# Kernel optimization log

Measured on AMD Instinct MI355X. Metric: run time of the kernel, lower is better.

## Reference

```python
import jax, jax.numpy as jnp
import numpy as np

BC = 48
DIM = 192


def setup_inputs() -> dict:
    key = jax.random.key(0)
    ks = jax.random.split(key, 10)
    s = 0.05
    return {
        "input": jax.random.normal(ks[0], (1, BC, DIM, DIM), jnp.float32),
        "qw": jax.random.normal(ks[1], (BC // 3, BC), jnp.float32) * s,
        "qb": jax.random.normal(ks[2], (BC // 3,), jnp.float32) * s,
        "kw": jax.random.normal(ks[3], (BC // 3, BC), jnp.float32) * s,
        "kb": jax.random.normal(ks[4], (BC // 3,), jnp.float32) * s,
        "vw": jax.random.normal(ks[5], (BC, BC), jnp.float32) * s,
        "vb": jax.random.normal(ks[6], (BC,), jnp.float32) * s,
        "gamma": jnp.float32(0.1),  # torch init is 0.0; nonzero to exercise attn path
        "dw": jax.random.normal(ks[7], (BC, BC, 4, 4), jnp.float32) * s,  # torch ConvTranspose2d [in,out,kh,kw]
        "db": jax.random.normal(ks[8], (BC,), jnp.float32) * s,
    }


def reference(input, qw, qb, kw, kb, vw, vb, gamma, dw, db):
    B, C, H, W = input.shape  # B == 1
    x = input.reshape(B, C, H // 2, 2, W // 2, 2).mean(axis=(3, 5))
    h, w = H // 2, W // 2
    n = h * w
    f = x.reshape(1, C, n)
    # 1x1 Conv1d == per-position linear over channels
    q = jnp.einsum('oc,bcn->bno', qw, f) + qb            # [1, N, bc//3]
    k = jnp.einsum('oc,bcn->bon', kw, f) + kb[:, None]    # [1, bc//3, N]
    v = jnp.einsum('oc,bcn->bon', vw, f) + vb[:, None]    # [1, bc, N]
    qk = jnp.einsum('bno,bom->bnm', q, k)                 # [1, N, N]
    attn = jax.nn.softmax(qk, axis=1)                     # softmax over QUERY axis (dim 1), as in source
    o = jnp.einsum('bcn,bnm->bcm', v, attn)               # [1, bc, N]
    out = gamma * o.reshape(x.shape) + x
    # ConvTranspose2d(k=4, s=2, p=1): conv with lhs_dilation=2, pad k-1-p=2, flipped kernel
    kern = jnp.flip(jnp.transpose(dw, (1, 0, 2, 3)), axis=(2, 3))  # [out, in, kh, kw]
    y = jax.lax.conv_general_dilated(
        out, kern, window_strides=(1, 1), padding=((2, 2), (2, 2)),
        lhs_dilation=(2, 2), dimension_numbers=('NCHW', 'OIHW', 'NCHW'))
    return y + db[None, :, None, None]
```

## Files before the change

### kernel.cpp

```cpp
#include <hip/hip_runtime.h>
#include <hip/hip_bf16.h>

#define C 48
#define HH 192
#define WW 192
#define HP 96
#define WP 96
#define NP 9216

#define OFF_QB    0
#define OFF_KB    36864
#define OFF_VT2   73728
#define OFF_PART  368640
#define OFF_XT    5087232
#define OFF_XTP   5529600
#define OFF_WB    5836928
#define WS_NEED_BYTES ((size_t)5861504 * 4)

typedef __attribute__((ext_vector_type(4))) short s16x4;
typedef __attribute__((ext_vector_type(8))) short s16x8;
typedef __attribute__((ext_vector_type(4))) float f32x4;

#if __has_builtin(__builtin_amdgcn_mfma_f32_16x16x16bf16_1k)
static __device__ inline f32x4 mfma16(s16x4 a, s16x4 b, f32x4 c) {
    return __builtin_amdgcn_mfma_f32_16x16x16bf16_1k(a, b, c, 0, 0, 0);
}
#else
static __device__ inline f32x4 mfma16(s16x4 a, s16x4 b, f32x4 c) {
    asm volatile("v_mfma_f32_16x16x16_bf16 %0, %1, %2, %0" : "+v"(c) : "v"(a), "v"(b));
    return c;
}
#endif

static __device__ inline f32x4 mfma32(s16x8 a, s16x8 b, f32x4 c) {
    return __builtin_amdgcn_mfma_f32_16x16x32_bf16(a, b, c, 0, 0, 0);
}

static __device__ inline float fexp2(float x) {
    float r;
    asm("v_exp_f32 %0, %1" : "=v"(r) : "v"(x));
    return r;
}

static __device__ inline unsigned short f2bf(float f) {
    union { float f; unsigned u; } v; v.f = f;
    unsigned r = v.u + 0x7fff + ((v.u >> 16) & 1);
    return (unsigned short)(r >> 16);
}

static __device__ inline float bf2f(unsigned short u) {
    union { unsigned u; float f; } v; v.u = ((unsigned)u) << 16; return v.f;
}

static __device__ inline s16x4 pack_bf16x4(float a, float b, float c, float d) {
    __hip_bfloat162 h0 = __float22bfloat162_rn(make_float2(a, b));
    __hip_bfloat162 h1 = __float22bfloat162_rn(make_float2(c, d));
    union { unsigned u[2]; s16x4 v; } pu;
    pu.u[0] = *reinterpret_cast<unsigned*>(&h0);
    pu.u[1] = *reinterpret_cast<unsigned*>(&h1);
    return pu.v;
}

__global__ void pool_k(const float* __restrict__ in, float* __restrict__ xT) {
    int idx = blockIdx.x * 256 + threadIdx.x;
    if (idx >= C * NP) return;
    int c = idx / NP, r = idx % NP;
    int y = r / WP, xx = r % WP;
    const float* p = in + (size_t)c * HH * WW + (2 * y) * WW + 2 * xx;
    xT[(size_t)r * 48 + c] = 0.25f * (p[0] + p[1] + p[WW] + p[WW + 1]);
}

__global__ void qkvprep_k(const float* __restrict__ xT,
                          const float* __restrict__ qw, const float* __restrict__ qb,
                          const float* __restrict__ kw, const float* __restrict__ kb,
                          const float* __restrict__ vw, const float* __restrict__ vb,
                          unsigned short* __restrict__ QB, unsigned short* __restrict__ KB,
                          unsigned short* __restrict__ VT2) {
    int tid = blockIdx.x * 256 + threadIdx.x;
    int p = tid % NP;
    int g = tid / NP;
    float f[C];
#pragma unroll
    for (int c4 = 0; c4 < C; c4 += 4) {
        f32x4 v = *(const f32x4*)(xT + (size_t)p * 48 + c4);
        f[c4] = v[0]; f[c4 + 1] = v[1]; f[c4 + 2] = v[2]; f[c4 + 3] = v[3];
    }
    int nt = p >> 4, nn = p & 15;
    if (g == 0) {
#pragma unroll
        for (int o = 0; o < 16; ++o) {
            float a = qb[o];
#pragma unroll
            for (int c = 0; c < C; ++c) a += qw[o * C + c] * f[c];
            QB[p * 16 + o] = f2bf(a);
        }
    } else if (g == 1) {
        const float L2E = 1.4426950408889634f;
#pragma unroll
        for (int o = 0; o < 16; ++o) {
            float a = kb[o];
#pragma unroll
            for (int c = 0; c < C; ++c) a += kw[o * C + c] * f[c];
            KB[p * 16 + o] = f2bf(a * L2E);
        }
        VT2[(size_t)nt * 1024 + 48 * 16 + nn] = 0x3F80;
#pragma unroll
        for (int r = 49; r < 64; ++r) VT2[(size_t)nt * 1024 + r * 16 + nn] = 0;
    } else {
        int c0 = (g - 2) * 16;
#pragma unroll
        for (int oo = 0; oo < 16; ++oo) {
            int o = c0 + oo;
            float a = vb[o];
#pragma unroll
            for (int c = 0; c < C; ++c) a += vw[o * C + c] * f[c];
            VT2[(size_t)nt * 1024 + o * 16 + nn] = f2bf(a);
        }
    }
}

#define MBLKS 72
#define NSPL  16
#define NSTEP 36

static __device__ __forceinline__ void attn_core(const unsigned short* __restrict__ QB,
                                                 const unsigned short* __restrict__ VT2,
                                                 s16x4 bq0, s16x4 bq1, int n0, int lo, int hi,
                                                 f32x4 o0[4], f32x4 o1[4]) {
    const unsigned short* qp = QB + (size_t)(n0 + lo) * 16 + 4 * hi;
    const unsigned short* vp = VT2 + (size_t)(n0 >> 4) * 1024 + lo * 16 + 4 * hi;

    s16x4 aq  = *(const s16x4*)qp;
    s16x4 bv0 = *(const s16x4*)(vp);
    s16x4 bv1 = *(const s16x4*)(vp + 256);
    s16x4 bv2 = *(const s16x4*)(vp + 512);
    s16x4 bv3 = *(const s16x4*)(vp + 768);

    for (int s = 0; s < NSTEP; ++s) {
        qp += 16 * 16;
        vp += 1024;
        s16x4 aqn  = *(const s16x4*)qp;
        s16x4 bvn0 = *(const s16x4*)(vp);
        s16x4 bvn1 = *(const s16x4*)(vp + 256);
        s16x4 bvn2 = *(const s16x4*)(vp + 512);
        s16x4 bvn3 = *(const s16x4*)(vp + 768);

        f32x4 z = {0.f, 0.f, 0.f, 0.f};
        f32x4 t0 = mfma16(aq, bq0, z);
        f32x4 t1 = mfma16(aq, bq1, z);

        s16x4 p0 = pack_bf16x4(fexp2(t0[0]), fexp2(t0[1]), fexp2(t0[2]), fexp2(t0[3]));
        s16x4 p1 = pack_bf16x4(fexp2(t1[0]), fexp2(t1[1]), fexp2(t1[2]), fexp2(t1[3]));

        o0[0] = mfma16(p0, bv0, o0[0]);
        o0[1] = mfma16(p0, bv1, o0[1]);
        o0[2] = mfma16(p0, bv2, o0[2]);
        o0[3] = mfma16(p0, bv3, o0[3]);
        o1[0] = mfma16(p1, bv0, o1[0]);
        o1[1] = mfma16(p1, bv1, o1[1]);
        o1[2] = mfma16(p1, bv2, o1[2]);
        o1[3] = mfma16(p1, bv3, o1[3]);

        aq = aqn; bv0 = bvn0; bv1 = bvn1; bv2 = bvn2; bv3 = bvn3;
    }
}

__global__ __launch_bounds__(256) void attn_k(const unsigned short* __restrict__ QB,
                                              const unsigned short* __restrict__ KB,
                                              const unsigned short* __restrict__ VT2,
                                              unsigned short* __restrict__ PART) {
    const int lane = threadIdx.x & 63;
    const int lo = lane & 15, hi = lane >> 4;
    const int wv = threadIdx.x >> 6;
    const int mblk = blockIdx.x % MBLKS;
    const int nspl = blockIdx.x / MBLKS;
    const int mt0 = mblk * 128 + wv * 32;

    const s16x4 bq0 = *(const s16x4*)(KB + (size_t)(mt0 + lo) * 16 + 4 * hi);
    const s16x4 bq1 = *(const s16x4*)(KB + (size_t)(mt0 + 16 + lo) * 16 + 4 * hi);

    f32x4 o0[4], o1[4];
#pragma unroll
    for (int i = 0; i < 4; ++i) {
        o0[i] = (f32x4){0.f, 0.f, 0.f, 0.f};
        o1[i] = (f32x4){0.f, 0.f, 0.f, 0.f};
    }
    attn_core(QB, VT2, bq0, bq1, nspl * (NP / NSPL), lo, hi, o0, o1);

    unsigned short* cp = PART + ((size_t)(mblk * 4 + wv) * NSPL + nspl) * 2048;
#pragma unroll
    for (int q = 0; q < 8; ++q) {
        const f32x4& o = (q >> 2) ? o1[q & 3] : o0[q & 3];
        s16x4 pk = pack_bf16x4(o[0], o[1], o[2], o[3]);
        *(s16x4*)(cp + q * 256 + lane * 4) = pk;
    }
}

__global__ __launch_bounds__(256) void reduce_epi_k(const unsigned short* __restrict__ PART,
                                                    const float* __restrict__ xT,
                                                    const float* __restrict__ gamma,
                                                    unsigned short* __restrict__ XTP) {
    __shared__ float sden[32];
    const int T = blockIdx.x;
    const int mt0 = (T >> 2) * 128 + (T & 3) * 32;
    const unsigned short* base = PART + (size_t)T * NSPL * 2048;
    const int t = threadIdx.x;

    if (t < 8) {
        int h = t >> 2, hi = t & 3;
        int idx = (h * 4 + 3) * 256 + (hi * 16) * 4;
        float a0 = 0.f, a1 = 0.f, a2 = 0.f, a3 = 0.f;
        for (int ns = 0; ns < NSPL; ++ns) {
            s16x4 v = *(const s16x4*)(base + ns * 2048 + idx);
            a0 += bf2f((unsigned short)v[0]);
            a1 += bf2f((unsigned short)v[1]);
            a2 += bf2f((unsigned short)v[2]);
            a3 += bf2f((unsigned short)v[3]);
        }
        sden[h * 16 + hi * 4 + 0] = a0;
        sden[h * 16 + hi * 4 + 1] = a1;
        sden[h * 16 + hi * 4 + 2] = a2;
        sden[h * 16 + hi * 4 + 3] = a3;
    }
    __syncthreads();

    float gam = gamma[0];
#pragma unroll
    for (int g = t; g < 512; g += 256) {
        int q = g >> 6, lane = g & 63;
        int h = q >> 2, ct = q & 3;
        int hi = lane >> 4, lo = lane & 15;
        int c = ct * 16 + lo;
        int idx = q * 256 + lane * 4;
        float a0 = 0.f, a1 = 0.f, a2 = 0.f, a3 = 0.f;
        for (int ns = 0; ns < NSPL; ++ns) {
            s16x4 v = *(const s16x4*)(base + ns * 2048 + idx);
            a0 += bf2f((unsigned short)v[0]);
            a1 += bf2f((unsigned short)v[1]);
            a2 += bf2f((unsigned short)v[2]);
            a3 += bf2f((unsigned short)v[3]);
        }
        if (c < 48) {
            float av[4] = {a0, a1, a2, a3};
#pragma unroll
            for (int j = 0; j < 4; ++j) {
                int ml = h * 16 + hi * 4 + j;
                int m = mt0 + ml;
                float val = gam * av[j] / sden[ml] + xT[(size_t)m * 48 + c];
                int iy = m / WP, ix = m % WP;
                XTP[((size_t)(iy + 1) * 98 + ix + 1) * 64 + c] = f2bf(val);
            }
        }
    }
}

__global__ __launch_bounds__(256) void attn_atomic_k(const unsigned short* __restrict__ QB,
                                                     const unsigned short* __restrict__ KB,
                                                     const unsigned short* __restrict__ VT2,
                                                     float* __restrict__ O4) {
    const int lane = threadIdx.x & 63;
    const int lo = lane & 15, hi = lane >> 4;
    const int wv = threadIdx.x >> 6;
    const int mblk = blockIdx.x % MBLKS;
    const int nspl = blockIdx.x / MBLKS;
    const int mt0 = mblk * 128 + wv * 32;

    const s16x4 bq0 = *(const s16x4*)(KB + (size_t)(mt0 + lo) * 16 + 4 * hi);
    const s16x4 bq1 = *(const s16x4*)(KB + (size_t)(mt0 + 16 + lo) * 16 + 4 * hi);

    f32x4 o0[4], o1[4];
#pragma unroll
    for (int i = 0; i < 4; ++i) {
        o0[i] = (f32x4){0.f, 0.f, 0.f, 0.f};
        o1[i] = (f32x4){0.f, 0.f, 0.f, 0.f};
    }
    attn_core(QB, VT2, bq0, bq1, nspl * (NP / NSPL), lo, hi, o0, o1);

    float* Oc = O4 + (size_t)(nspl & 3) * (NP * 64);
#pragma unroll
    for (int ct = 0; ct < 4; ++ct)
#pragma unroll
        for (int j = 0; j < 4; ++j) {
            atomicAdd(&Oc[(size_t)(mt0 + 4 * hi + j) * 64 + 16 * ct + lo], o0[ct][j]);
            atomicAdd(&Oc[(size_t)(mt0 + 16 + 4 * hi + j) * 64 + 16 * ct + lo], o1[ct][j]);
        }
}

__global__ void epi_atomic_k(const float* __restrict__ O4, const float* __restrict__ xT,
                             const float* __restrict__ gamma, unsigned short* __restrict__ XTP) {
    int m = blockIdx.x * 256 + threadIdx.x;
    if (m >= NP) return;
    int iy = m / WP, ix = m % WP;
    unsigned short* xp = XTP + ((size_t)(iy + 1) * 98 + ix + 1) * 64;
    float den = 0.f;
#pragma unroll
    for (int cp = 0; cp < 4; ++cp) den += O4[(size_t)cp * (NP * 64) + (size_t)m * 64 + 48];
    float rg = gamma[0] / den;
#pragma unroll
    for (int c = 0; c < C; ++c) {
        float o = 0.f;
#pragma unroll
        for (int cp = 0; cp < 4; ++cp) o += O4[(size_t)cp * (NP * 64) + (size_t)m * 64 + c];
        xp[c] = f2bf(rg * o + xT[(size_t)m * 48 + c]);
    }
}

__global__ void wprep_k(const float* __restrict__ dw, unsigned short* __restrict__ WB) {
    int idx = blockIdx.x * 256 + threadIdx.x;
    if (idx >= 16 * 48 * 64) return;
    int ci = idx & 63;
    int co = (idx >> 6) % 48;
    int kidx = idx / (48 * 64);
    float v = (ci < C) ? dw[((size_t)ci * C + co) * 16 + kidx] : 0.f;
    WB[idx] = f2bf(v);
}

__global__ __launch_bounds__(128) void convt_mfma_k(const unsigned short* __restrict__ XTP,
                                                    const unsigned short* __restrict__ WB,
                                                    const float* __restrict__ db,
                                                    float* __restrict__ y) {
    const int lane = threadIdx.x & 63;
    const int lo = lane & 15, hi = lane >> 4;
    const int wv = threadIdx.x >> 6;
    const int b = blockIdx.x;
    const int oyp = b >> 2;
    const int py = (b >> 1) & 1;
    const int px = b & 1;

    const int sy[2] = {0, py ? 1 : -1};
    const int kyt[2] = {py ? 2 : 1, py ? 0 : 3};
    const int sx[2] = {0, px ? 1 : -1};
    const int kxt[2] = {px ? 2 : 1, px ? 0 : 3};

    s16x8 bw[2][2][2][3];
#pragma unroll
    for (int ty = 0; ty < 2; ++ty)
#pragma unroll
        for (int tx = 0; tx < 2; ++tx) {
            const unsigned short* wp = WB + (size_t)(kyt[ty] * 4 + kxt[tx]) * 48 * 64;
#pragma unroll
            for (int kk = 0; kk < 2; ++kk)
#pragma unroll
                for (int ct = 0; ct < 3; ++ct)
                    bw[ty][tx][kk][ct] = *(const s16x8*)(wp + (size_t)(ct * 16 + lo) * 64 + kk * 32 + 8 * hi);
        }
    float bias[3];
#pragma unroll
    for (int ct = 0; ct < 3; ++ct) bias[ct] = db[ct * 16 + lo];

    const int oy = 2 * oyp + py;
    for (int i = 0; i < 3; ++i) {
        int ox0 = (wv * 3 + i) * 16;
        f32x4 acc[3];
#pragma unroll
        for (int ct = 0; ct < 3; ++ct) acc[ct] = (f32x4){bias[ct], bias[ct], bias[ct], bias[ct]};
#pragma unroll
        for (int ty = 0; ty < 2; ++ty) {
            int R0 = (oyp + sy[ty] + 1) * 98;
#pragma unroll
            for (int tx = 0; tx < 2; ++tx) {
                const unsigned short* ap = XTP + (size_t)(R0 + ox0 + sx[tx] + 1 + lo) * 64 + 8 * hi;
#pragma unroll
                for (int kk = 0; kk < 2; ++kk) {
                    s16x8 a = *(const s16x8*)(ap + kk * 32);
                    acc[0] = mfma32(a, bw[ty][tx][kk][0], acc[0]);
                    acc[1] = mfma32(a, bw[ty][tx][kk][1], acc[1]);
                    acc[2] = mfma32(a, bw[ty][tx][kk][2], acc[2]);
                }
            }
        }
#pragma unroll
        for (int ct = 0; ct < 3; ++ct)
#pragma unroll
            for (int j = 0; j < 4; ++j)
                y[(size_t)(ct * 16 + lo) * (HH * WW) + oy * WW + 2 * (ox0 + 4 * hi + j) + px] = acc[ct][j];
    }
}

extern "C" void kernel_launch(void* const* d_in, const int* in_sizes, int n_in,
                              void* d_out, int out_size, void* d_ws, size_t ws_size,
                              hipStream_t stream) {
    const float* in    = (const float*)d_in[0];
    const float* qw    = (const float*)d_in[1];
    const float* qb    = (const float*)d_in[2];
    const float* kw    = (const float*)d_in[3];
    const float* kb    = (const float*)d_in[4];
    const float* vw    = (const float*)d_in[5];
    const float* vb    = (const float*)d_in[6];
    const float* gamma = (const float*)d_in[7];
    const float* dw    = (const float*)d_in[8];
    const float* db    = (const float*)d_in[9];
    float* out = (float*)d_out;

    float* ws = (float*)d_ws;
    unsigned short* QB   = (unsigned short*)(ws + OFF_QB);
    unsigned short* KB   = (unsigned short*)(ws + OFF_KB);
    unsigned short* VT2  = (unsigned short*)(ws + OFF_VT2);
    unsigned short* PART = (unsigned short*)(ws + OFF_PART);
    float*          xT   = ws + OFF_XT;
    unsigned short* XTP  = (unsigned short*)(ws + OFF_XTP);
    unsigned short* WB   = (unsigned short*)(ws + OFF_WB);

    pool_k<<<(C * NP + 255) / 256, 256, 0, stream>>>(in, xT);
    qkvprep_k<<<(5 * NP) / 256, 256, 0, stream>>>(xT, qw, qb, kw, kb, vw, vb, QB, KB, VT2);
    hipMemsetAsync(XTP, 0, (size_t)98 * 98 * 64 * sizeof(unsigned short), stream);
    wprep_k<<<(16 * 48 * 64) / 256, 256, 0, stream>>>(dw, WB);

    if (ws_size >= WS_NEED_BYTES) {
        attn_k<<<MBLKS * NSPL, 256, 0, stream>>>(QB, KB, VT2, PART);
        reduce_epi_k<<<288, 256, 0, stream>>>(PART, xT, gamma, XTP);
    } else {
        float* O4 = (float*)PART;
        hipMemsetAsync(O4, 0, (size_t)4 * NP * 64 * sizeof(float), stream);
        attn_atomic_k<<<MBLKS * NSPL, 256, 0, stream>>>(QB, KB, VT2, O4);
        epi_atomic_k<<<(NP + 255) / 256, 256, 0, stream>>>(O4, xT, gamma, XTP);
    }
    convt_mfma_k<<<96 * 2 * 2, 128, 0, stream>>>(XTP, WB, db, out);
}
```

Baseline: 85.98 us.

## Widen attention tiles to 64 keys per wave and zero only XTP border

The attention kernel now has each wave cover 64 key positions (four 16-row tiles) instead of 32, so every Q/V fragment it loads feeds twice as many MFMAs. The query range is split 32 ways instead of 16, and the reduction kernel is reshaped to match (144 blocks over 64 positions each). The full memset of the padded XTP buffer is replaced by writing zeros only to its one-pixel border inside wprep_k. In exchange it uses twice the accumulator registers, which may lower occupancy, and needs a larger partials buffer, so the atomic fallback runs when the workspace is too small.

```diff
diff --git a/kernel.cpp b/kernel.cpp
--- a/kernel.cpp
+++ b/kernel.cpp
@@ -11,11 +11,12 @@
 #define OFF_QB    0
 #define OFF_KB    36864
 #define OFF_VT2   73728
-#define OFF_PART  368640
-#define OFF_XT    5087232
-#define OFF_XTP   5529600
-#define OFF_WB    5836928
-#define WS_NEED_BYTES ((size_t)5861504 * 4)
+#define OFF_XT    368640
+#define OFF_XTP   811008
+#define OFF_WB    1118336
+#define OFF_PART  1142912
+#define WS_NEED_BYTES ((size_t)10580096 * 4)
+#define FB_NEED_BYTES ((size_t)3502208 * 4)
 
 typedef __attribute__((ext_vector_type(4))) short s16x4;
 typedef __attribute__((ext_vector_type(8))) short s16x8;
@@ -119,51 +120,9 @@
     }
 }
 
-#define MBLKS 72
-#define NSPL  16
-#define NSTEP 36
-
-static __device__ __forceinline__ void attn_core(const unsigned short* __restrict__ QB,
-                                                 const unsigned short* __restrict__ VT2,
-                                                 s16x4 bq0, s16x4 bq1, int n0, int lo, int hi,
-                                                 f32x4 o0[4], f32x4 o1[4]) {
-    const unsigned short* qp = QB + (size_t)(n0 + lo) * 16 + 4 * hi;
-    const unsigned short* vp = VT2 + (size_t)(n0 >> 4) * 1024 + lo * 16 + 4 * hi;
-
-    s16x4 aq  = *(const s16x4*)qp;
-    s16x4 bv0 = *(const s16x4*)(vp);
-    s16x4 bv1 = *(const s16x4*)(vp + 256);
-    s16x4 bv2 = *(const s16x4*)(vp + 512);
-    s16x4 bv3 = *(const s16x4*)(vp + 768);
-
-    for (int s = 0; s < NSTEP; ++s) {
-        qp += 16 * 16;
-        vp += 1024;
-        s16x4 aqn  = *(const s16x4*)qp;
-        s16x4 bvn0 = *(const s16x4*)(vp);
-        s16x4 bvn1 = *(const s16x4*)(vp + 256);
-        s16x4 bvn2 = *(const s16x4*)(vp + 512);
-        s16x4 bvn3 = *(const s16x4*)(vp + 768);
-
-        f32x4 z = {0.f, 0.f, 0.f, 0.f};
-        f32x4 t0 = mfma16(aq, bq0, z);
-        f32x4 t1 = mfma16(aq, bq1, z);
-
-        s16x4 p0 = pack_bf16x4(fexp2(t0[0]), fexp2(t0[1]), fexp2(t0[2]), fexp2(t0[3]));
-        s16x4 p1 = pack_bf16x4(fexp2(t1[0]), fexp2(t1[1]), fexp2(t1[2]), fexp2(t1[3]));
-
-        o0[0] = mfma16(p0, bv0, o0[0]);
-        o0[1] = mfma16(p0, bv1, o0[1]);
-        o0[2] = mfma16(p0, bv2, o0[2]);
-        o0[3] = mfma16(p0, bv3, o0[3]);
-        o1[0] = mfma16(p1, bv0, o1[0]);
-        o1[1] = mfma16(p1, bv1, o1[1]);
-        o1[2] = mfma16(p1, bv2, o1[2]);
-        o1[3] = mfma16(p1, bv3, o1[3]);
-
-        aq = aqn; bv0 = bvn0; bv1 = bvn1; bv2 = bvn2; bv3 = bvn3;
-    }
-}
+#define MBLKS 36
+#define NSPL  32
+#define NSTEP 18
 
 __global__ __launch_bounds__(256) void attn_k(const unsigned short* __restrict__ QB,
                                               const unsigned short* __restrict__ KB,
@@ -174,67 +133,119 @@
     const int wv = threadIdx.x >> 6;
     const int mblk = blockIdx.x % MBLKS;
     const int nspl = blockIdx.x / MBLKS;
-    const int mt0 = mblk * 128 + wv * 32;
-
-    const s16x4 bq0 = *(const s16x4*)(KB + (size_t)(mt0 + lo) * 16 + 4 * hi);
-    const s16x4 bq1 = *(const s16x4*)(KB + (size_t)(mt0 + 16 + lo) * 16 + 4 * hi);
-
-    f32x4 o0[4], o1[4];
-#pragma unroll
-    for (int i = 0; i < 4; ++i) {
-        o0[i] = (f32x4){0.f, 0.f, 0.f, 0.f};
-        o1[i] = (f32x4){0.f, 0.f, 0.f, 0.f};
-    }
-    attn_core(QB, VT2, bq0, bq1, nspl * (NP / NSPL), lo, hi, o0, o1);
-
-    unsigned short* cp = PART + ((size_t)(mblk * 4 + wv) * NSPL + nspl) * 2048;
-#pragma unroll
-    for (int q = 0; q < 8; ++q) {
-        const f32x4& o = (q >> 2) ? o1[q & 3] : o0[q & 3];
-        s16x4 pk = pack_bf16x4(o[0], o[1], o[2], o[3]);
-        *(s16x4*)(cp + q * 256 + lane * 4) = pk;
-    }
+    const int mt0 = mblk * 256 + wv * 64;
+
+    s16x4 bq0 = *(const s16x4*)(KB + (size_t)(mt0 + lo) * 16 + 4 * hi);
+    s16x4 bq1 = *(const s16x4*)(KB + (size_t)(mt0 + 16 + lo) * 16 + 4 * hi);
+    s16x4 bq2 = *(const s16x4*)(KB + (size_t)(mt0 + 32 + lo) * 16 + 4 * hi);
+    s16x4 bq3 = *(const s16x4*)(KB + (size_t)(mt0 + 48 + lo) * 16 + 4 * hi);
+
+    f32x4 o[4][4];
+#pragma unroll
+    for (int mt = 0; mt < 4; ++mt)
+#pragma unroll
+        for (int ct = 0; ct < 4; ++ct) o[mt][ct] = (f32x4){0.f, 0.f, 0.f, 0.f};
+
+    const int n0 = nspl * (NP / NSPL);
+    const unsigned short* qp = QB + (size_t)(n0 + lo) * 16 + 4 * hi;
+    const unsigned short* vp = VT2 + (size_t)(n0 >> 4) * 1024 + lo * 16 + 4 * hi;
+
+    s16x4 aq  = *(const s16x4*)qp;
+    s16x4 bv0 = *(const s16x4*)(vp);
+    s16x4 bv1 = *(const s16x4*)(vp + 256);
+    s16x4 bv2 = *(const s16x4*)(vp + 512);
+    s16x4 bv3 = *(const s16x4*)(vp + 768);
+
+    for (int s = 0; s < NSTEP; ++s) {
+        qp += 256;
+        vp += 1024;
+        s16x4 aqn  = *(const s16x4*)qp;
+        s16x4 bvn0 = *(const s16x4*)(vp);
+        s16x4 bvn1 = *(const s16x4*)(vp + 256);
+        s16x4 bvn2 = *(const s16x4*)(vp + 512);
+        s16x4 bvn3 = *(const s16x4*)(vp + 768);
+
+        f32x4 z = {0.f, 0.f, 0.f, 0.f};
+        f32x4 t0 = mfma16(aq, bq0, z);
+        f32x4 t1 = mfma16(aq, bq1, z);
+        f32x4 t2 = mfma16(aq, bq2, z);
+        f32x4 t3 = mfma16(aq, bq3, z);
+
+        s16x4 p0 = pack_bf16x4(fexp2(t0[0]), fexp2(t0[1]), fexp2(t0[2]), fexp2(t0[3]));
+        s16x4 p1 = pack_bf16x4(fexp2(t1[0]), fexp2(t1[1]), fexp2(t1[2]), fexp2(t1[3]));
+        s16x4 p2 = pack_bf16x4(fexp2(t2[0]), fexp2(t2[1]), fexp2(t2[2]), fexp2(t2[3]));
+        s16x4 p3 = pack_bf16x4(fexp2(t3[0]), fexp2(t3[1]), fexp2(t3[2]), fexp2(t3[3]));
+
+        o[0][0] = mfma16(p0, bv0, o[0][0]);
+        o[0][1] = mfma16(p0, bv1, o[0][1]);
+        o[0][2] = mfma16(p0, bv2, o[0][2]);
+        o[0][3] = mfma16(p0, bv3, o[0][3]);
+        o[1][0] = mfma16(p1, bv0, o[1][0]);
+        o[1][1] = mfma16(p1, bv1, o[1][1]);
+        o[1][2] = mfma16(p1, bv2, o[1][2]);
+        o[1][3] = mfma16(p1, bv3, o[1][3]);
+        o[2][0] = mfma16(p2, bv0, o[2][0]);
+        o[2][1] = mfma16(p2, bv1, o[2][1]);
+        o[2][2] = mfma16(p2, bv2, o[2][2]);
+        o[2][3] = mfma16(p2, bv3, o[2][3]);
+        o[3][0] = mfma16(p3, bv0, o[3][0]);
+        o[3][1] = mfma16(p3, bv1, o[3][1]);
+        o[3][2] = mfma16(p3, bv2, o[3][2]);
+        o[3][3] = mfma16(p3, bv3, o[3][3]);
+
+        aq = aqn; bv0 = bvn0; bv1 = bvn1; bv2 = bvn2; bv3 = bvn3;
+    }
+
+    unsigned short* cp = PART + ((size_t)(mblk * 4 + wv) * NSPL + nspl) * 4096;
+#pragma unroll
+    for (int mt = 0; mt < 4; ++mt)
+#pragma unroll
+        for (int ct = 0; ct < 4; ++ct) {
+            int q = mt * 4 + ct;
+            s16x4 pk = pack_bf16x4(o[mt][ct][0], o[mt][ct][1], o[mt][ct][2], o[mt][ct][3]);
+            *(s16x4*)(cp + q * 256 + lane * 4) = pk;
+        }
 }
 
 __global__ __launch_bounds__(256) void reduce_epi_k(const unsigned short* __restrict__ PART,
                                                     const float* __restrict__ xT,
                                                     const float* __restrict__ gamma,
                                                     unsigned short* __restrict__ XTP) {
-    __shared__ float sden[32];
+    __shared__ float sden[64];
     const int T = blockIdx.x;
-    const int mt0 = (T >> 2) * 128 + (T & 3) * 32;
-    const unsigned short* base = PART + (size_t)T * NSPL * 2048;
+    const int mt0 = T * 64;
+    const unsigned short* base = PART + (size_t)T * NSPL * 4096;
     const int t = threadIdx.x;
 
-    if (t < 8) {
-        int h = t >> 2, hi = t & 3;
-        int idx = (h * 4 + 3) * 256 + (hi * 16) * 4;
+    if (t < 16) {
+        int mt = t >> 2, hi = t & 3;
+        int idx = (mt * 4 + 3) * 256 + hi * 64;
         float a0 = 0.f, a1 = 0.f, a2 = 0.f, a3 = 0.f;
         for (int ns = 0; ns < NSPL; ++ns) {
-            s16x4 v = *(const s16x4*)(base + ns * 2048 + idx);
+            s16x4 v = *(const s16x4*)(base + ns * 4096 + idx);
             a0 += bf2f((unsigned short)v[0]);
             a1 += bf2f((unsigned short)v[1]);
             a2 += bf2f((unsigned short)v[2]);
             a3 += bf2f((unsigned short)v[3]);
         }
-        sden[h * 16 + hi * 4 + 0] = a0;
-        sden[h * 16 + hi * 4 + 1] = a1;
-        sden[h * 16 + hi * 4 + 2] = a2;
-        sden[h * 16 + hi * 4 + 3] = a3;
+        sden[mt * 16 + hi * 4 + 0] = a0;
+        sden[mt * 16 + hi * 4 + 1] = a1;
+        sden[mt * 16 + hi * 4 + 2] = a2;
+        sden[mt * 16 + hi * 4 + 3] = a3;
     }
     __syncthreads();
 
     float gam = gamma[0];
 #pragma unroll
-    for (int g = t; g < 512; g += 256) {
-        int q = g >> 6, lane = g & 63;
-        int h = q >> 2, ct = q & 3;
-        int hi = lane >> 4, lo = lane & 15;
+    for (int g = 0; g < 4; ++g) {
+        int q = g * 4 + (t >> 6);
+        int mt = q >> 2, ct = q & 3;
+        int hi = (t >> 4) & 3, lo = t & 15;
         int c = ct * 16 + lo;
-        int idx = q * 256 + lane * 4;
+        int idx = q * 256 + (t & 63) * 4;
         float a0 = 0.f, a1 = 0.f, a2 = 0.f, a3 = 0.f;
         for (int ns = 0; ns < NSPL; ++ns) {
-            s16x4 v = *(const s16x4*)(base + ns * 2048 + idx);
+            s16x4 v = *(const s16x4*)(base + ns * 4096 + idx);
             a0 += bf2f((unsigned short)v[0]);
             a1 += bf2f((unsigned short)v[1]);
             a2 += bf2f((unsigned short)v[2]);
@@ -244,13 +255,49 @@
             float av[4] = {a0, a1, a2, a3};
 #pragma unroll
             for (int j = 0; j < 4; ++j) {
-                int ml = h * 16 + hi * 4 + j;
+                int ml = mt * 16 + hi * 4 + j;
                 int m = mt0 + ml;
                 float val = gam * av[j] / sden[ml] + xT[(size_t)m * 48 + c];
                 int iy = m / WP, ix = m % WP;
                 XTP[((size_t)(iy + 1) * 98 + ix + 1) * 64 + c] = f2bf(val);
             }
         }
+    }
+}
+
+static __device__ __forceinline__ void attn_core32(const unsigned short* __restrict__ QB,
+                                                   const unsigned short* __restrict__ VT2,
+                                                   s16x4 bq0, s16x4 bq1, int n0, int lo, int hi,
+                                                   f32x4 o0[4], f32x4 o1[4]) {
+    const unsigned short* qp = QB + (size_t)(n0 + lo) * 16 + 4 * hi;
+    const unsigned short* vp = VT2 + (size_t)(n0 >> 4) * 1024 + lo * 16 + 4 * hi;
+    s16x4 aq  = *(const s16x4*)qp;
+    s16x4 bv0 = *(const s16x4*)(vp);
+    s16x4 bv1 = *(const s16x4*)(vp + 256);
+    s16x4 bv2 = *(const s16x4*)(vp + 512);
+    s16x4 bv3 = *(const s16x4*)(vp + 768);
+    for (int s = 0; s < NSTEP; ++s) {
+        qp += 256;
+        vp += 1024;
+        s16x4 aqn  = *(const s16x4*)qp;
+        s16x4 bvn0 = *(const s16x4*)(vp);
+        s16x4 bvn1 = *(const s16x4*)(vp + 256);
+        s16x4 bvn2 = *(const s16x4*)(vp + 512);
+        s16x4 bvn3 = *(const s16x4*)(vp + 768);
+        f32x4 z = {0.f, 0.f, 0.f, 0.f};
+        f32x4 t0 = mfma16(aq, bq0, z);
+        f32x4 t1 = mfma16(aq, bq1, z);
+        s16x4 p0 = pack_bf16x4(fexp2(t0[0]), fexp2(t0[1]), fexp2(t0[2]), fexp2(t0[3]));
+        s16x4 p1 = pack_bf16x4(fexp2(t1[0]), fexp2(t1[1]), fexp2(t1[2]), fexp2(t1[3]));
+        o0[0] = mfma16(p0, bv0, o0[0]);
+        o0[1] = mfma16(p0, bv1, o0[1]);
+        o0[2] = mfma16(p0, bv2, o0[2]);
+        o0[3] = mfma16(p0, bv3, o0[3]);
+        o1[0] = mfma16(p1, bv0, o1[0]);
+        o1[1] = mfma16(p1, bv1, o1[1]);
+        o1[2] = mfma16(p1, bv2, o1[2]);
+        o1[3] = mfma16(p1, bv3, o1[3]);
+        aq = aqn; bv0 = bvn0; bv1 = bvn1; bv2 = bvn2; bv3 = bvn3;
     }
 }
 
@@ -261,21 +308,18 @@
     const int lane = threadIdx.x & 63;
     const int lo = lane & 15, hi = lane >> 4;
     const int wv = threadIdx.x >> 6;
-    const int mblk = blockIdx.x % MBLKS;
-    const int nspl = blockIdx.x / MBLKS;
+    const int mblk = blockIdx.x % 72;
+    const int nspl = blockIdx.x / 72;
     const int mt0 = mblk * 128 + wv * 32;
-
     const s16x4 bq0 = *(const s16x4*)(KB + (size_t)(mt0 + lo) * 16 + 4 * hi);
     const s16x4 bq1 = *(const s16x4*)(KB + (size_t)(mt0 + 16 + lo) * 16 + 4 * hi);
-
     f32x4 o0[4], o1[4];
 #pragma unroll
     for (int i = 0; i < 4; ++i) {
         o0[i] = (f32x4){0.f, 0.f, 0.f, 0.f};
         o1[i] = (f32x4){0.f, 0.f, 0.f, 0.f};
     }
-    attn_core(QB, VT2, bq0, bq1, nspl * (NP / NSPL), lo, hi, o0, o1);
-
+    attn_core32(QB, VT2, bq0, bq1, nspl * 288, lo, hi, o0, o1);
     float* Oc = O4 + (size_t)(nspl & 3) * (NP * 64);
 #pragma unroll
     for (int ct = 0; ct < 4; ++ct)
@@ -305,8 +349,19 @@
     }
 }
 
-__global__ void wprep_k(const float* __restrict__ dw, unsigned short* __restrict__ WB) {
+__global__ void wprep_k(const float* __restrict__ dw, unsigned short* __restrict__ WB,
+                        unsigned short* __restrict__ XTP) {
     int idx = blockIdx.x * 256 + threadIdx.x;
+    if (idx < 3104) {
+        int pos = idx >> 3, cc = (idx & 7) * 8;
+        int row, col;
+        if (pos < 98)       { row = 0;             col = pos; }
+        else if (pos < 196) { row = 97;            col = pos - 98; }
+        else if (pos < 292) { row = pos - 196 + 1; col = 0; }
+        else                { row = pos - 292 + 1; col = 97; }
+        s16x8 zz = (s16x8){0, 0, 0, 0, 0, 0, 0, 0};
+        *(s16x8*)(XTP + ((size_t)row * 98 + col) * 64 + cc) = zz;
+    }
     if (idx >= 16 * 48 * 64) return;
     int ci = idx & 63;
     int co = (idx >> 6) % 48;
@@ -396,23 +451,22 @@
     unsigned short* QB   = (unsigned short*)(ws + OFF_QB);
     unsigned short* KB   = (unsigned short*)(ws + OFF_KB);
     unsigned short* VT2  = (unsigned short*)(ws + OFF_VT2);
-    unsigned short* PART = (unsigned short*)(ws + OFF_PART);
     float*          xT   = ws + OFF_XT;
     unsigned short* XTP  = (unsigned short*)(ws + OFF_XTP);
     unsigned short* WB   = (unsigned short*)(ws + OFF_WB);
+    unsigned short* PART = (unsigned short*)(ws + OFF_PART);
 
     pool_k<<<(C * NP + 255) / 256, 256, 0, stream>>>(in, xT);
     qkvprep_k<<<(5 * NP) / 256, 256, 0, stream>>>(xT, qw, qb, kw, kb, vw, vb, QB, KB, VT2);
-    hipMemsetAsync(XTP, 0, (size_t)98 * 98 * 64 * sizeof(unsigned short), stream);
-    wprep_k<<<(16 * 48 * 64) / 256, 256, 0, stream>>>(dw, WB);
+    wprep_k<<<(16 * 48 * 64) / 256, 256, 0, stream>>>(dw, WB, XTP);
 
     if (ws_size >= WS_NEED_BYTES) {
         attn_k<<<MBLKS * NSPL, 256, 0, stream>>>(QB, KB, VT2, PART);
-        reduce_epi_k<<<288, 256, 0, stream>>>(PART, xT, gamma, XTP);
+        reduce_epi_k<<<144, 256, 0, stream>>>(PART, xT, gamma, XTP);
     } else {
         float* O4 = (float*)PART;
         hipMemsetAsync(O4, 0, (size_t)4 * NP * 64 * sizeof(float), stream);
-        attn_atomic_k<<<MBLKS * NSPL, 256, 0, stream>>>(QB, KB, VT2, O4);
+        attn_atomic_k<<<72 * 32, 256, 0, stream>>>(QB, KB, VT2, O4);
         epi_atomic_k<<<(NP + 255) / 256, 256, 0, stream>>>(O4, xT, gamma, XTP);
     }
     convt_mfma_k<<<96 * 2 * 2, 128, 0, stream>>>(XTP, WB, db, out);
```

Result: slower. 93.73 us (+9.0%).

## Double attention split count, split conv-transpose blocks, fuse XTP border zeroing

Applied to the files above, without the earlier changes.

Raises the number of key-axis splits in the attention kernel from 16 to 32, halving the steps per block and doubling grid size so more waves run in parallel. The conv-transpose kernel is split three ways per row so each block handles one 16-wide tile instead of looping over three. The full memset of the padded XTP buffer is replaced by zeroing only its border inside the weight-prep kernel. The price is a larger partial-sum buffer and a heavier reduction pass, and the workspace requirement nearly doubles, which may push execution onto the atomic fallback path.

```diff
diff --git a/kernel.cpp b/kernel.cpp
--- a/kernel.cpp
+++ b/kernel.cpp
@@ -11,11 +11,11 @@
 #define OFF_QB    0
 #define OFF_KB    36864
 #define OFF_VT2   73728
-#define OFF_PART  368640
-#define OFF_XT    5087232
-#define OFF_XTP   5529600
-#define OFF_WB    5836928
-#define WS_NEED_BYTES ((size_t)5861504 * 4)
+#define OFF_XT    368640
+#define OFF_XTP   811008
+#define OFF_WB    1118336
+#define OFF_PART  1142912
+#define WS_NEED_BYTES ((size_t)10580096 * 4)
 
 typedef __attribute__((ext_vector_type(4))) short s16x4;
 typedef __attribute__((ext_vector_type(8))) short s16x8;
@@ -120,38 +120,33 @@
 }
 
 #define MBLKS 72
-#define NSPL  16
-#define NSTEP 36
-
-static __device__ __forceinline__ void attn_core(const unsigned short* __restrict__ QB,
-                                                 const unsigned short* __restrict__ VT2,
-                                                 s16x4 bq0, s16x4 bq1, int n0, int lo, int hi,
-                                                 f32x4 o0[4], f32x4 o1[4]) {
+#define NSPL  32
+#define NSTEP 18
+
+static __device__ __forceinline__ void attn_core32(const unsigned short* __restrict__ QB,
+                                                   const unsigned short* __restrict__ VT2,
+                                                   s16x4 bq0, s16x4 bq1, int n0, int lo, int hi,
+                                                   f32x4 o0[4], f32x4 o1[4]) {
     const unsigned short* qp = QB + (size_t)(n0 + lo) * 16 + 4 * hi;
     const unsigned short* vp = VT2 + (size_t)(n0 >> 4) * 1024 + lo * 16 + 4 * hi;
-
     s16x4 aq  = *(const s16x4*)qp;
     s16x4 bv0 = *(const s16x4*)(vp);
     s16x4 bv1 = *(const s16x4*)(vp + 256);
     s16x4 bv2 = *(const s16x4*)(vp + 512);
     s16x4 bv3 = *(const s16x4*)(vp + 768);
-
     for (int s = 0; s < NSTEP; ++s) {
-        qp += 16 * 16;
+        qp += 256;
         vp += 1024;
         s16x4 aqn  = *(const s16x4*)qp;
         s16x4 bvn0 = *(const s16x4*)(vp);
         s16x4 bvn1 = *(const s16x4*)(vp + 256);
         s16x4 bvn2 = *(const s16x4*)(vp + 512);
         s16x4 bvn3 = *(const s16x4*)(vp + 768);
-
         f32x4 z = {0.f, 0.f, 0.f, 0.f};
         f32x4 t0 = mfma16(aq, bq0, z);
         f32x4 t1 = mfma16(aq, bq1, z);
-
         s16x4 p0 = pack_bf16x4(fexp2(t0[0]), fexp2(t0[1]), fexp2(t0[2]), fexp2(t0[3]));
         s16x4 p1 = pack_bf16x4(fexp2(t1[0]), fexp2(t1[1]), fexp2(t1[2]), fexp2(t1[3]));
-
         o0[0] = mfma16(p0, bv0, o0[0]);
         o0[1] = mfma16(p0, bv1, o0[1]);
         o0[2] = mfma16(p0, bv2, o0[2]);
@@ -160,7 +155,6 @@
         o1[1] = mfma16(p1, bv1, o1[1]);
         o1[2] = mfma16(p1, bv2, o1[2]);
         o1[3] = mfma16(p1, bv3, o1[3]);
-
         aq = aqn; bv0 = bvn0; bv1 = bvn1; bv2 = bvn2; bv3 = bvn3;
     }
 }
@@ -185,7 +179,7 @@
         o0[i] = (f32x4){0.f, 0.f, 0.f, 0.f};
         o1[i] = (f32x4){0.f, 0.f, 0.f, 0.f};
     }
-    attn_core(QB, VT2, bq0, bq1, nspl * (NP / NSPL), lo, hi, o0, o1);
+    attn_core32(QB, VT2, bq0, bq1, nspl * (NP / NSPL), lo, hi, o0, o1);
 
     unsigned short* cp = PART + ((size_t)(mblk * 4 + wv) * NSPL + nspl) * 2048;
 #pragma unroll
@@ -261,21 +255,18 @@
     const int lane = threadIdx.x & 63;
     const int lo = lane & 15, hi = lane >> 4;
     const int wv = threadIdx.x >> 6;
-    const int mblk = blockIdx.x % MBLKS;
-    const int nspl = blockIdx.x / MBLKS;
+    const int mblk = blockIdx.x % 72;
+    const int nspl = blockIdx.x / 72;
     const int mt0 = mblk * 128 + wv * 32;
-
     const s16x4 bq0 = *(const s16x4*)(KB + (size_t)(mt0 + lo) * 16 + 4 * hi);
     const s16x4 bq1 = *(const s16x4*)(KB + (size_t)(mt0 + 16 + lo) * 16 + 4 * hi);
-
     f32x4 o0[4], o1[4];
 #pragma unroll
     for (int i = 0; i < 4; ++i) {
         o0[i] = (f32x4){0.f, 0.f, 0.f, 0.f};
         o1[i] = (f32x4){0.f, 0.f, 0.f, 0.f};
     }
-    attn_core(QB, VT2, bq0, bq1, nspl * (NP / NSPL), lo, hi, o0, o1);
-
+    attn_core32(QB, VT2, bq0, bq1, nspl * 288, lo, hi, o0, o1);
     float* Oc = O4 + (size_t)(nspl & 3) * (NP * 64);
 #pragma unroll
     for (int ct = 0; ct < 4; ++ct)
@@ -305,8 +296,19 @@
     }
 }
 
-__global__ void wprep_k(const float* __restrict__ dw, unsigned short* __restrict__ WB) {
+__global__ void wprep_k(const float* __restrict__ dw, unsigned short* __restrict__ WB,
+                        unsigned short* __restrict__ XTP) {
     int idx = blockIdx.x * 256 + threadIdx.x;
+    if (idx < 3104) {
+        int pos = idx >> 3, cc = (idx & 7) * 8;
+        int row, col;
+        if (pos < 98)       { row = 0;             col = pos; }
+        else if (pos < 196) { row = 97;            col = pos - 98; }
+        else if (pos < 292) { row = pos - 196 + 1; col = 0; }
+        else                { row = pos - 292 + 1; col = 97; }
+        s16x8 zz = (s16x8){0, 0, 0, 0, 0, 0, 0, 0};
+        *(s16x8*)(XTP + ((size_t)row * 98 + col) * 64 + cc) = zz;
+    }
     if (idx >= 16 * 48 * 64) return;
     int ci = idx & 63;
     int co = (idx >> 6) % 48;
@@ -323,9 +325,11 @@
     const int lo = lane & 15, hi = lane >> 4;
     const int wv = threadIdx.x >> 6;
     const int b = blockIdx.x;
-    const int oyp = b >> 2;
-    const int py = (b >> 1) & 1;
-    const int px = b & 1;
+    const int i3 = b % 3;
+    const int r3 = b / 3;
+    const int px = r3 & 1;
+    const int py = (r3 >> 1) & 1;
+    const int oyp = r3 >> 2;
 
     const int sy[2] = {0, py ? 1 : -1};
     const int kyt[2] = {py ? 2 : 1, py ? 0 : 3};
@@ -349,32 +353,30 @@
     for (int ct = 0; ct < 3; ++ct) bias[ct] = db[ct * 16 + lo];
 
     const int oy = 2 * oyp + py;
-    for (int i = 0; i < 3; ++i) {
-        int ox0 = (wv * 3 + i) * 16;
-        f32x4 acc[3];
-#pragma unroll
-        for (int ct = 0; ct < 3; ++ct) acc[ct] = (f32x4){bias[ct], bias[ct], bias[ct], bias[ct]};
-#pragma unroll
-        for (int ty = 0; ty < 2; ++ty) {
-            int R0 = (oyp + sy[ty] + 1) * 98;
-#pragma unroll
-            for (int tx = 0; tx < 2; ++tx) {
-                const unsigned short* ap = XTP + (size_t)(R0 + ox0 + sx[tx] + 1 + lo) * 64 + 8 * hi;
-#pragma unroll
-                for (int kk = 0; kk < 2; ++kk) {
-                    s16x8 a = *(const s16x8*)(ap + kk * 32);
-                    acc[0] = mfma32(a, bw[ty][tx][kk][0], acc[0]);
-                    acc[1] = mfma32(a, bw[ty][tx][kk][1], acc[1]);
-                    acc[2] = mfma32(a, bw[ty][tx][kk][2], acc[2]);
-                }
+    const int ox0 = (wv * 3 + i3) * 16;
+    f32x4 acc[3];
+#pragma unroll
+    for (int ct = 0; ct < 3; ++ct) acc[ct] = (f32x4){bias[ct], bias[ct], bias[ct], bias[ct]};
+#pragma unroll
+    for (int ty = 0; ty < 2; ++ty) {
+        int R0 = (oyp + sy[ty] + 1) * 98;
+#pragma unroll
+        for (int tx = 0; tx < 2; ++tx) {
+            const unsigned short* ap = XTP + (size_t)(R0 + ox0 + sx[tx] + 1 + lo) * 64 + 8 * hi;
+#pragma unroll
+            for (int kk = 0; kk < 2; ++kk) {
+                s16x8 a = *(const s16x8*)(ap + kk * 32);
+                acc[0] = mfma32(a, bw[ty][tx][kk][0], acc[0]);
+                acc[1] = mfma32(a, bw[ty][tx][kk][1], acc[1]);
+                acc[2] = mfma32(a, bw[ty][tx][kk][2], acc[2]);
             }
         }
-#pragma unroll
-        for (int ct = 0; ct < 3; ++ct)
-#pragma unroll
-            for (int j = 0; j < 4; ++j)
-                y[(size_t)(ct * 16 + lo) * (HH * WW) + oy * WW + 2 * (ox0 + 4 * hi + j) + px] = acc[ct][j];
-    }
+    }
+#pragma unroll
+    for (int ct = 0; ct < 3; ++ct)
+#pragma unroll
+        for (int j = 0; j < 4; ++j)
+            y[(size_t)(ct * 16 + lo) * (HH * WW) + oy * WW + 2 * (ox0 + 4 * hi + j) + px] = acc[ct][j];
 }
 
 extern "C" void kernel_launch(void* const* d_in, const int* in_sizes, int n_in,
@@ -396,15 +398,14 @@
     unsigned short* QB   = (unsigned short*)(ws + OFF_QB);
     unsigned short* KB   = (unsigned short*)(ws + OFF_KB);
     unsigned short* VT2  = (unsigned short*)(ws + OFF_VT2);
-    unsigned short* PART = (unsigned short*)(ws + OFF_PART);
     float*          xT   = ws + OFF_XT;
     unsigned short* XTP  = (unsigned short*)(ws + OFF_XTP);
     unsigned short* WB   = (unsigned short*)(ws + OFF_WB);
+    unsigned short* PART = (unsigned short*)(ws + OFF_PART);
 
     pool_k<<<(C * NP + 255) / 256, 256, 0, stream>>>(in, xT);
     qkvprep_k<<<(5 * NP) / 256, 256, 0, stream>>>(xT, qw, qb, kw, kb, vw, vb, QB, KB, VT2);
-    hipMemsetAsync(XTP, 0, (size_t)98 * 98 * 64 * sizeof(unsigned short), stream);
-    wprep_k<<<(16 * 48 * 64) / 256, 256, 0, stream>>>(dw, WB);
+    wprep_k<<<(16 * 48 * 64) / 256, 256, 0, stream>>>(dw, WB, XTP);
 
     if (ws_size >= WS_NEED_BYTES) {
         attn_k<<<MBLKS * NSPL, 256, 0, stream>>>(QB, KB, VT2, PART);
@@ -412,8 +413,8 @@
     } else {
         float* O4 = (float*)PART;
         hipMemsetAsync(O4, 0, (size_t)4 * NP * 64 * sizeof(float), stream);
-        attn_atomic_k<<<MBLKS * NSPL, 256, 0, stream>>>(QB, KB, VT2, O4);
+        attn_atomic_k<<<72 * 32, 256, 0, stream>>>(QB, KB, VT2, O4);
         epi_atomic_k<<<(NP + 255) / 256, 256, 0, stream>>>(O4, xT, gamma, XTP);
     }
-    convt_mfma_k<<<96 * 2 * 2, 128, 0, stream>>>(XTP, WB, db, out);
-}
+    convt_mfma_k<<<96 * 2 * 2 * 3, 128, 0, stream>>>(XTP, WB, db, out);
+}
```

After: 86.53 us. Within noise of the previous version (+0.6%).
